# Performance work log

Measured on AMD Instinct MI355X. Metric: run time of the kernel, lower is better.

The kernel has to match this reference:

```python
import jax, jax.numpy as jnp
import numpy as np

D_MODEL = 1024
NUM_HEADS = 16
DEPTH = D_MODEL // NUM_HEADS


def setup_inputs() -> dict:
    key = jax.random.key(0)
    ks = jax.random.split(key, 11)
    B, S = 4, 2048
    scale = 1.0 / np.sqrt(D_MODEL)
    inp = {
        "q": jax.random.normal(ks[0], (B, S, D_MODEL), jnp.float32),
        "k": jax.random.normal(ks[1], (B, S, D_MODEL), jnp.float32),
        "v": jax.random.normal(ks[2], (B, S, D_MODEL), jnp.float32),
        # Linear params (weight stored [out, in] like torch; applied as x @ W.T + b)
        "wq_w": jax.random.normal(ks[3], (D_MODEL, D_MODEL), jnp.float32) * scale,
        "wq_b": jnp.zeros((D_MODEL,), jnp.float32),
        "wk_w": jax.random.normal(ks[4], (D_MODEL, D_MODEL), jnp.float32) * scale,
        "wk_b": jnp.zeros((D_MODEL,), jnp.float32),
        "wv_w": jax.random.normal(ks[5], (D_MODEL, D_MODEL), jnp.float32) * scale,
        "wv_b": jnp.zeros((D_MODEL,), jnp.float32),
        "wo_w": jax.random.normal(ks[6], (D_MODEL, D_MODEL), jnp.float32) * scale,
        "wo_b": jnp.zeros((D_MODEL,), jnp.float32),
    }
    return inp


def _split_heads(x, B, S):
    # [B, S, D] -> [B, H, S, depth]
    return x.reshape(B, S, NUM_HEADS, DEPTH).transpose(0, 2, 1, 3)


def reference(q, k, v, wq_w, wq_b, wk_w, wk_b, wv_w, wv_b, wo_w, wo_b):
    B, S, _ = q.shape
    qh = _split_heads(q @ wq_w.T + wq_b, B, S)
    kh = _split_heads(k @ wk_w.T + wk_b, B, S)
    vh = _split_heads(v @ wv_w.T + wv_b, B, S)
    # scaled dot-product attention: [B, H, Sq, Sk]
    scores = jnp.einsum("bhqd,bhkd->bhqk", qh, kh) / jnp.sqrt(
        jnp.asarray(DEPTH, qh.dtype))
    attn = jax.nn.softmax(scores, axis=-1)
    ctx = jnp.einsum("bhqk,bhkd->bhqd", attn, vh)
    # [B, H, S, depth] -> [B, S, D]
    ctx = ctx.transpose(0, 2, 1, 3).reshape(B, S, D_MODEL)
    return ctx @ wo_w.T + wo_b
```

## Files before the change

### kernel.cpp

```cpp
#include <hip/hip_runtime.h>
#include <hip/hip_bf16.h>

typedef __attribute__((ext_vector_type(8))) short bf16x8;
typedef __attribute__((ext_vector_type(4))) short bf16x4;
typedef __attribute__((ext_vector_type(4))) float f32x4;
typedef __attribute__((address_space(3))) ushort lds_ushort;

#define MFMA32(a, b, c) __builtin_amdgcn_mfma_f32_16x16x32_bf16(a, b, c, 0, 0, 0)
#if __has_builtin(__builtin_amdgcn_mfma_f32_16x16x16bf16_1k)
#define HAVE_MFMA16K 1
#define MFMA16K(a, b, c) __builtin_amdgcn_mfma_f32_16x16x16bf16_1k(a, b, c, 0, 0, 0)
#else
#define HAVE_MFMA16K 0
#endif

#define ASYNC16(g, l)                                                          \
    __builtin_amdgcn_global_load_lds(                                          \
        (const __attribute__((address_space(1))) unsigned int*)(g),            \
        (__attribute__((address_space(3))) unsigned int*)(l), 16, 0, 0)

#define TR16(dst, addr, OFF)                                                   \
    asm volatile("ds_read_b64_tr_b16 %0, %1 offset:%2"                         \
                 : "=v"(dst) : "v"(addr), "i"(OFF))

__device__ __forceinline__ ushort f2bf(float f) {
    __hip_bfloat16 h = __float2bfloat16(f);
    return *reinterpret_cast<ushort*>(&h);
}
__device__ __forceinline__ uint pack_bf16_2(float a, float b) {
    uint ua = __float_as_uint(a) + 0x8000u;
    uint ub = __float_as_uint(b) + 0x8000u;
    return (ua >> 16) | (ub & 0xFFFF0000u);
}

#define QSCALE 0.18033688011112042f

struct CvtArgs { const float* s[7]; ushort* d[7]; int nb[7]; };

__global__ __launch_bounds__(256) void cvtk(CvtArgs a) {
    const int z = blockIdx.y;
    if ((int)blockIdx.x >= a.nb[z]) return;
    const float* s = a.s[z];
    ushort* d = a.d[z];
    const size_t i = (size_t)blockIdx.x * 2048 + threadIdx.x * 8;
    float4 f0 = *(const float4*)&s[i];
    float4 f1 = *(const float4*)&s[i + 4];
    *(ushort4*)&d[i]     = make_ushort4(f2bf(f0.x), f2bf(f0.y), f2bf(f0.z), f2bf(f0.w));
    *(ushort4*)&d[i + 4] = make_ushort4(f2bf(f1.x), f2bf(f1.y), f2bf(f1.z), f2bf(f1.w));
}

struct GemmArgs {
    const ushort* X[3]; const ushort* W[3]; const float* B[3];
    void* O[3]; int mode[3]; float scale[3];
};

__global__ __launch_bounds__(256) void gemm3(GemmArgs g) {
    __shared__ __attribute__((aligned(16))) ushort As[2][128][32];
    __shared__ __attribute__((aligned(16))) ushort Bs[2][128][32];

    const int z = blockIdx.z;
    const ushort* __restrict__ X = g.X[z];
    const ushort* __restrict__ W = g.W[z];
    const float*  __restrict__ bias = g.B[z];
    const int mode = g.mode[z];
    const float scale = g.scale[z];

    const int tid  = threadIdx.x;
    const int lane = tid & 63;
    const int wave = tid >> 6;
    const int quad = lane >> 4;
    const int l16  = lane & 15;
    const int wm   = (wave >> 1) * 64;
    const int wn   = (wave & 1) * 64;

    const int flat = blockIdx.x + 8 * blockIdx.y;
    const int t    = (flat & 7) * 64 + (flat >> 3);
    const int m0   = (t >> 3) * 128;
    const int n0   = (t & 7) * 128;

    f32x4 acc[4][4];
#pragma unroll
    for (int i = 0; i < 4; i++)
#pragma unroll
        for (int j = 0; j < 4; j++) acc[i][j] = (f32x4)0.0f;

    auto stage = [&](int buf, int k0) {
#pragma unroll
        for (int j = 0; j < 2; j++) {
            const int c   = j * 256 + tid;
            const int r   = c >> 2;
            const int col = (c & 3) * 8;
            ASYNC16(&X[(size_t)(m0 + r) * 1024 + k0 + col],
                    &As[buf][0][0] + (size_t)(j * 256 + wave * 64) * 8);
            ASYNC16(&W[(size_t)(n0 + r) * 1024 + k0 + col],
                    &Bs[buf][0][0] + (size_t)(j * 256 + wave * 64) * 8);
        }
    };

    stage(0, 0);
    int cur = 0;

    for (int k0 = 0; k0 < 1024; k0 += 32) {
        __syncthreads();
        if (k0 + 32 < 1024) stage(cur ^ 1, k0 + 32);

        bf16x8 af[4], bfr[4];
#pragma unroll
        for (int i = 0; i < 4; i++)
            af[i] = *(const bf16x8*)&As[cur][wm + i * 16 + l16][quad * 8];
#pragma unroll
        for (int j = 0; j < 4; j++)
            bfr[j] = *(const bf16x8*)&Bs[cur][wn + j * 16 + l16][quad * 8];
#pragma unroll
        for (int i = 0; i < 4; i++)
#pragma unroll
            for (int j = 0; j < 4; j++)
                acc[i][j] = MFMA32(af[i], bfr[j], acc[i][j]);
        cur ^= 1;
    }

#pragma unroll
    for (int i = 0; i < 4; i++) {
#pragma unroll
        for (int j = 0; j < 4; j++) {
            const int n  = n0 + wn + j * 16 + l16;
            const float bb = bias[n];
#pragma unroll
            for (int r = 0; r < 4; r++) {
                const int m = m0 + wm + i * 16 + quad * 4 + r;
                const float val = (acc[i][j][r] + bb) * scale;
                if (mode == 2) {
                    ((float*)g.O[z])[(size_t)m * 1024 + n] = val;
                } else {
                    const int bat = m >> 11, s = m & 2047, h = n >> 6, d = n & 63;
                    ((ushort*)g.O[z])[((size_t)((bat * 16 + h) * 2048 + s)) * 64 + d]
                        = f2bf(val);
                }
            }
        }
    }
}

__global__ __launch_bounds__(256, 4) void attn(
    const ushort* __restrict__ Qp, const ushort* __restrict__ Kp,
    const ushort* __restrict__ Vp, ushort* __restrict__ ctx)
{
    __shared__ __attribute__((aligned(16))) ushort Ks[2][2 * 64 * 32];
    __shared__ __attribute__((aligned(16))) ushort Vs[2][64 * 64];

    const int tid  = threadIdx.x;
    const int lane = tid & 63;
    const int wave = tid >> 6;
    const int quad = lane >> 4;
    const int l16  = lane & 15;

    const int id = blockIdx.x;
    const int bh = (id & 7) * 8 + ((id >> 3) & 7);
    const int q0 = (id >> 6) * 128;
    const int b  = bh >> 4, h = bh & 15;

    const ushort* Qg = Qp + ((size_t)bh * 2048 + q0) * 64;
    const ushort* Kg = Kp + (size_t)bh * 2048 * 64;
    const ushort* Vg = Vp + (size_t)bh * 2048 * 64;

    bf16x8 aq[2][2];
#pragma unroll
    for (int st = 0; st < 2; st++)
#pragma unroll
        for (int kk = 0; kk < 2; kk++)
            aq[st][kk] = *(const bf16x8*)&Qg[(size_t)(wave * 32 + st * 16 + l16) * 64
                                            + kk * 32 + quad * 8];

    f32x4 o[2][4];
#pragma unroll
    for (int st = 0; st < 2; st++)
#pragma unroll
        for (int jd = 0; jd < 4; jd++) o[st][jd] = (f32x4)0.0f;
    float lsum[2] = {0.f, 0.f};

    auto stage = [&](int buf, int n0) {
#pragma unroll
        for (int j = 0; j < 2; j++) {
            const int c    = j * 256 + tid;
            const int colq = c & 3;
            const int row  = (c >> 2) & 63;
            const int half = c >> 8;
            ASYNC16(&Kg[(size_t)(n0 + row) * 64 + half * 32 + colq * 8],
                    &Ks[buf][0] + (size_t)(j * 256 + wave * 64) * 8);
        }
#pragma unroll
        for (int j = 0; j < 2; j++) {
            const int c   = j * 256 + tid;
            const int key = ((c >> 5) << 2) | ((c >> 1) & 3);
            const int d   = (((c >> 3) & 3) << 4) | ((c & 1) << 3);
            ASYNC16(&Vg[(size_t)(n0 + key) * 64 + d],
                    &Vs[buf][0] + (size_t)(j * 256 + wave * 64) * 8);
        }
    };

    stage(0, 0);
    int cur = 0;

    for (int n0 = 0; n0 < 2048; n0 += 64) {
        __syncthreads();
        if (n0 + 64 < 2048) stage(cur ^ 1, n0 + 64);

        uint pk[4][2][2];
#pragma unroll
        for (int kb = 0; kb < 4; kb++) {
            bf16x8 kf0 = *(const bf16x8*)&Ks[cur][(size_t)(kb * 16 + l16) * 32 + quad * 8];
            bf16x8 kf1 = *(const bf16x8*)&Ks[cur][(size_t)(64 + kb * 16 + l16) * 32 + quad * 8];
#pragma unroll
            for (int st = 0; st < 2; st++) {
                f32x4 s = (f32x4)0.0f;
                s = MFMA32(kf0, aq[st][0], s);
                s = MFMA32(kf1, aq[st][1], s);
                float e0 = __builtin_amdgcn_exp2f(s[0]);
                float e1 = __builtin_amdgcn_exp2f(s[1]);
                float e2 = __builtin_amdgcn_exp2f(s[2]);
                float e3 = __builtin_amdgcn_exp2f(s[3]);
                lsum[st] += (e0 + e1) + (e2 + e3);
                pk[kb][st][0] = pack_bf16_2(e0, e1);
                pk[kb][st][1] = pack_bf16_2(e2, e3);
            }
        }

#if HAVE_MFMA16K
        const lds_ushort* vp = (const lds_ushort*)&Vs[cur][0] + quad * 256 + l16 * 4;
        bf16x4 vf[4][4];
#define TRISSUE(JD)                                                            \
        TR16(vf[JD][0], vp, (JD) * 128 + 0);                                   \
        TR16(vf[JD][1], vp, (JD) * 128 + 2048);                                \
        TR16(vf[JD][2], vp, (JD) * 128 + 4096);                                \
        TR16(vf[JD][3], vp, (JD) * 128 + 6144);
        TRISSUE(0) TRISSUE(1) TRISSUE(2) TRISSUE(3)

#define PVWAIT(N)                                                              \
        asm volatile("s_waitcnt lgkmcnt(" #N ")" ::: "memory");                \
        __builtin_amdgcn_sched_barrier(0);
#define PVJD(JD)                                                               \
        _Pragma("unroll")                                                      \
        for (int kb = 0; kb < 4; kb++) {                                       \
            _Pragma("unroll")                                                  \
            for (int st = 0; st < 2; st++) {                                   \
                union { uint u[2]; bf16x4 v; } pf;                             \
                pf.u[0] = pk[kb][st][0];                                       \
                pf.u[1] = pk[kb][st][1];                                       \
                o[st][JD] = MFMA16K(pf.v, vf[JD][kb], o[st][JD]);              \
            }                                                                  \
        }
        __builtin_amdgcn_s_setprio(1);
        PVWAIT(12) PVJD(0)
        PVWAIT(8)  PVJD(1)
        PVWAIT(4)  PVJD(2)
        PVWAIT(0)  PVJD(3)
        __builtin_amdgcn_s_setprio(0);
#else
        const int addr0 = 4 * ((2 * (quad & 1)) * 16 + l16);
        const int addr1 = addr0 + 64;
#pragma unroll
        for (int kt = 0; kt < 2; kt++) {
            bf16x8 apf[2];
#pragma unroll
            for (int st = 0; st < 2; st++) {
                union { uint u[4]; bf16x8 v; } t;
#pragma unroll
                for (int j = 0; j < 4; j++) {
                    uint src = (quad & 2) ? pk[kt * 2 + 1][st][j & 1]
                                          : pk[kt * 2][st][j & 1];
                    t.u[j] = (uint)__builtin_amdgcn_ds_bpermute(
                        (j >> 1) ? addr1 : addr0, (int)src);
                }
                apf[st] = t.v;
            }
#pragma unroll
            for (int jd = 0; jd < 4; jd++) {
                union { ushort s[8]; bf16x8 v; } vv;
#pragma unroll
                for (int e = 0; e < 8; e++) {
                    const int key = kt * 32 + quad * 8 + e;
                    const int d   = jd * 16 + l16;
                    vv.s[e] = Vs[cur][(key >> 2) * 256 + (d >> 4) * 64
                                      + (key & 3) * 16 + (d & 15)];
                }
#pragma unroll
                for (int st = 0; st < 2; st++)
                    o[st][jd] = MFMA32(apf[st], vv.v, o[st][jd]);
            }
        }
#endif
        cur ^= 1;
    }

#pragma unroll
    for (int st = 0; st < 2; st++) {
        float ls = lsum[st];
        ls += __shfl_xor(ls, 16, 64);
        ls += __shfl_xor(ls, 32, 64);
        float inv[4];
#pragma unroll
        for (int r = 0; r < 4; r++)
            inv[r] = 1.0f / __shfl(ls, quad * 4 + r, 64);
#pragma unroll
        for (int jd = 0; jd < 4; jd++) {
#pragma unroll
            for (int r = 0; r < 4; r++) {
                const int s = q0 + wave * 32 + st * 16 + quad * 4 + r;
                ctx[((size_t)(b * 2048 + s)) * 1024 + h * 64 + jd * 16 + l16] =
                    f2bf(o[st][jd][r] * inv[r]);
            }
        }
    }
}

extern "C" void kernel_launch(void* const* d_in, const int* in_sizes, int n_in,
                              void* d_out, int out_size, void* d_ws, size_t ws_size,
                              hipStream_t stream) {
    const float* q    = (const float*)d_in[0];
    const float* k    = (const float*)d_in[1];
    const float* v    = (const float*)d_in[2];
    const float* wq_w = (const float*)d_in[3];
    const float* wq_b = (const float*)d_in[4];
    const float* wk_w = (const float*)d_in[5];
    const float* wk_b = (const float*)d_in[6];
    const float* wv_w = (const float*)d_in[7];
    const float* wv_b = (const float*)d_in[8];
    const float* wo_w = (const float*)d_in[9];
    const float* wo_b = (const float*)d_in[10];
    float* out = (float*)d_out;

    const size_t NE = (size_t)4 * 2048 * 1024;
    const size_t NW = (size_t)1024 * 1024;
    const size_t need_fused = (6 * NE + 4 * NW) * 2;

    dim3 blk(256);

    if (ws_size >= need_fused) {
        ushort* Xq = (ushort*)d_ws;
        ushort* Xk = Xq + NE;
        ushort* Xv = Xk + NE;
        ushort* Wq = Xv + NE;
        ushort* Wk = Wq + NW;
        ushort* Wv = Wk + NW;
        ushort* Wo = Wv + NW;
        ushort* Qp = Wo + NW;
        ushort* Kp = Qp + NE;
        ushort* Vp = Kp + NE;
        ushort* ctx = Xq;

        CvtArgs ca;
        ca.s[0]=q;    ca.d[0]=Xq; ca.nb[0]=4096;
        ca.s[1]=k;    ca.d[1]=Xk; ca.nb[1]=4096;
        ca.s[2]=v;    ca.d[2]=Xv; ca.nb[2]=4096;
        ca.s[3]=wq_w; ca.d[3]=Wq; ca.nb[3]=512;
        ca.s[4]=wk_w; ca.d[4]=Wk; ca.nb[4]=512;
        ca.s[5]=wv_w; ca.d[5]=Wv; ca.nb[5]=512;
        ca.s[6]=wo_w; ca.d[6]=Wo; ca.nb[6]=512;
        cvtk<<<dim3(4096, 7), blk, 0, stream>>>(ca);

        GemmArgs ga;
        ga.X[0]=Xq; ga.W[0]=Wq; ga.B[0]=wq_b; ga.O[0]=Qp; ga.mode[0]=0; ga.scale[0]=QSCALE;
        ga.X[1]=Xk; ga.W[1]=Wk; ga.B[1]=wk_b; ga.O[1]=Kp; ga.mode[1]=0; ga.scale[1]=1.0f;
        ga.X[2]=Xv; ga.W[2]=Wv; ga.B[2]=wv_b; ga.O[2]=Vp; ga.mode[2]=0; ga.scale[2]=1.0f;
        gemm3<<<dim3(8, 64, 3), blk, 0, stream>>>(ga);

        attn<<<dim3(1024), blk, 0, stream>>>(Qp, Kp, Vp, ctx);

        GemmArgs go;
        go.X[0]=ctx; go.W[0]=Wo; go.B[0]=wo_b; go.O[0]=out; go.mode[0]=2; go.scale[0]=1.0f;
        go.X[1]=go.X[0]; go.W[1]=go.W[0]; go.B[1]=go.B[0]; go.O[1]=go.O[0]; go.mode[1]=2; go.scale[1]=1.0f;
        go.X[2]=go.X[0]; go.W[2]=go.W[0]; go.B[2]=go.B[0]; go.O[2]=go.O[0]; go.mode[2]=2; go.scale[2]=1.0f;
        gemm3<<<dim3(8, 64, 1), blk, 0, stream>>>(go);
    } else {
        ushort* Xb  = (ushort*)d_ws;
        ushort* Wb  = Xb + NE;
        ushort* Wob = Wb + NW;
        ushort* Qp  = Wob + NW;
        ushort* Kp  = Qp + NE;
        ushort* Vp  = Kp + NE;
        ushort* ctx = Xb;

        CvtArgs c0;
        c0.s[0]=q;    c0.d[0]=Xb;  c0.nb[0]=4096;
        c0.s[1]=wq_w; c0.d[1]=Wb;  c0.nb[1]=512;
        c0.s[2]=wo_w; c0.d[2]=Wob; c0.nb[2]=512;
        for (int i = 3; i < 7; i++) { c0.s[i]=q; c0.d[i]=Xb; c0.nb[i]=0; }
        cvtk<<<dim3(4096, 3), blk, 0, stream>>>(c0);
        GemmArgs ga;
        for (int i = 0; i < 3; i++) { ga.X[i]=Xb; ga.W[i]=Wb; ga.B[i]=wq_b; ga.O[i]=Qp; ga.mode[i]=0; ga.scale[i]=QSCALE; }
        gemm3<<<dim3(8, 64, 1), blk, 0, stream>>>(ga);

        CvtArgs c1;
        c1.s[0]=k;    c1.d[0]=Xb; c1.nb[0]=4096;
        c1.s[1]=wk_w; c1.d[1]=Wb; c1.nb[1]=512;
        for (int i = 2; i < 7; i++) { c1.s[i]=k; c1.d[i]=Xb; c1.nb[i]=0; }
        cvtk<<<dim3(4096, 2), blk, 0, stream>>>(c1);
        GemmArgs gb;
        for (int i = 0; i < 3; i++) { gb.X[i]=Xb; gb.W[i]=Wb; gb.B[i]=wk_b; gb.O[i]=Kp; gb.mode[i]=0; gb.scale[i]=1.0f; }
        gemm3<<<dim3(8, 64, 1), blk, 0, stream>>>(gb);

        CvtArgs c2;
        c2.s[0]=v;    c2.d[0]=Xb; c2.nb[0]=4096;
        c2.s[1]=wv_w; c2.d[1]=Wb; c2.nb[1]=512;
        for (int i = 2; i < 7; i++) { c2.s[i]=v; c2.d[i]=Xb; c2.nb[i]=0; }
        cvtk<<<dim3(4096, 2), blk, 0, stream>>>(c2);
        GemmArgs gc;
        for (int i = 0; i < 3; i++) { gc.X[i]=Xb; gc.W[i]=Wb; gc.B[i]=wv_b; gc.O[i]=Vp; gc.mode[i]=0; gc.scale[i]=1.0f; }
        gemm3<<<dim3(8, 64, 1), blk, 0, stream>>>(gc);

        attn<<<dim3(1024), blk, 0, stream>>>(Qp, Kp, Vp, ctx);

        GemmArgs go;
        for (int i = 0; i < 3; i++) { go.X[i]=ctx; go.W[i]=Wob; go.B[i]=wo_b; go.O[i]=out; go.mode[i]=2; go.scale[i]=1.0f; }
        gemm3<<<dim3(8, 64, 1), blk, 0, stream>>>(go);
    }
}
```

Before: 350.8 us.

## Deepen GEMM prefetch pipeline, use MFMA for softmax row sums, hardware bf16 pack

The projection GEMM now prefetches two K-tiles ahead. It uses explicit vmcnt waits and split barriers so the next load is issued right after the fragments are read into registers, which should overlap global loads with MFMA compute. In the attention kernel, the softmax denominator is now accumulated with an MFMA against a ones vector instead of scalar adds and cross-lane shuffles. That MFMA sums the bf16-rounded probabilities, which slightly changes numerics. Packing the exponentials to bf16 now uses the v_cvt_pk_bf16_f32 instruction in place of the manual integer rounding.

```diff
diff --git a/kernel.cpp b/kernel.cpp
--- a/kernel.cpp
+++ b/kernel.cpp
@@ -27,10 +27,10 @@
     __hip_bfloat16 h = __float2bfloat16(f);
     return *reinterpret_cast<ushort*>(&h);
 }
-__device__ __forceinline__ uint pack_bf16_2(float a, float b) {
-    uint ua = __float_as_uint(a) + 0x8000u;
-    uint ub = __float_as_uint(b) + 0x8000u;
-    return (ua >> 16) | (ub & 0xFFFF0000u);
+__device__ __forceinline__ uint cvtpk(float a, float b) {
+    uint r;
+    asm("v_cvt_pk_bf16_f32 %0, %1, %2" : "=v"(r) : "v"(a), "v"(b));
+    return r;
 }
 
 #define QSCALE 0.18033688011112042f
@@ -98,11 +98,17 @@
     };
 
     stage(0, 0);
+    stage(1, 32);
     int cur = 0;
 
     for (int k0 = 0; k0 < 1024; k0 += 32) {
-        __syncthreads();
-        if (k0 + 32 < 1024) stage(cur ^ 1, k0 + 32);
+        if (k0 < 1024 - 32) {
+            asm volatile("s_waitcnt vmcnt(4)" ::: "memory");
+        } else {
+            asm volatile("s_waitcnt vmcnt(0)" ::: "memory");
+        }
+        __builtin_amdgcn_s_barrier();
+        __builtin_amdgcn_sched_barrier(0);
 
         bf16x8 af[4], bfr[4];
 #pragma unroll
@@ -111,6 +117,12 @@
 #pragma unroll
         for (int j = 0; j < 4; j++)
             bfr[j] = *(const bf16x8*)&Bs[cur][wn + j * 16 + l16][quad * 8];
+        asm volatile("s_waitcnt lgkmcnt(0)" ::: "memory");
+        __builtin_amdgcn_sched_barrier(0);
+        __builtin_amdgcn_s_barrier();
+        __builtin_amdgcn_sched_barrier(0);
+        if (k0 + 64 < 1024) stage(cur, k0 + 64);
+
 #pragma unroll
         for (int i = 0; i < 4; i++)
 #pragma unroll
@@ -176,7 +188,13 @@
     for (int st = 0; st < 2; st++)
 #pragma unroll
         for (int jd = 0; jd < 4; jd++) o[st][jd] = (f32x4)0.0f;
+#if HAVE_MFMA16K
+    f32x4 ls[2] = {(f32x4)0.0f, (f32x4)0.0f};
+    union { uint u[2]; bf16x4 v; } ones;
+    ones.u[0] = 0x3F803F80u; ones.u[1] = 0x3F803F80u;
+#else
     float lsum[2] = {0.f, 0.f};
+#endif
 
     auto stage = [&](int buf, int n0) {
 #pragma unroll
@@ -219,9 +237,11 @@
                 float e1 = __builtin_amdgcn_exp2f(s[1]);
                 float e2 = __builtin_amdgcn_exp2f(s[2]);
                 float e3 = __builtin_amdgcn_exp2f(s[3]);
+                pk[kb][st][0] = cvtpk(e0, e1);
+                pk[kb][st][1] = cvtpk(e2, e3);
+#if !HAVE_MFMA16K
                 lsum[st] += (e0 + e1) + (e2 + e3);
-                pk[kb][st][0] = pack_bf16_2(e0, e1);
-                pk[kb][st][1] = pack_bf16_2(e2, e3);
+#endif
             }
         }
 
@@ -234,6 +254,17 @@
         TR16(vf[JD][2], vp, (JD) * 128 + 4096);                                \
         TR16(vf[JD][3], vp, (JD) * 128 + 6144);
         TRISSUE(0) TRISSUE(1) TRISSUE(2) TRISSUE(3)
+
+#pragma unroll
+        for (int kb = 0; kb < 4; kb++) {
+#pragma unroll
+            for (int st = 0; st < 2; st++) {
+                union { uint u[2]; bf16x4 v; } pf;
+                pf.u[0] = pk[kb][st][0];
+                pf.u[1] = pk[kb][st][1];
+                ls[st] = MFMA16K(pf.v, ones.v, ls[st]);
+            }
+        }
 
 #define PVWAIT(N)                                                              \
         asm volatile("s_waitcnt lgkmcnt(" #N ")" ::: "memory");                \
@@ -292,15 +323,12 @@
         cur ^= 1;
     }
 
+#if HAVE_MFMA16K
 #pragma unroll
     for (int st = 0; st < 2; st++) {
-        float ls = lsum[st];
-        ls += __shfl_xor(ls, 16, 64);
-        ls += __shfl_xor(ls, 32, 64);
         float inv[4];
 #pragma unroll
-        for (int r = 0; r < 4; r++)
-            inv[r] = 1.0f / __shfl(ls, quad * 4 + r, 64);
+        for (int r = 0; r < 4; r++) inv[r] = 1.0f / ls[st][r];
 #pragma unroll
         for (int jd = 0; jd < 4; jd++) {
 #pragma unroll
@@ -311,6 +339,27 @@
             }
         }
     }
+#else
+#pragma unroll
+    for (int st = 0; st < 2; st++) {
+        float lsv = lsum[st];
+        lsv += __shfl_xor(lsv, 16, 64);
+        lsv += __shfl_xor(lsv, 32, 64);
+        float inv[4];
+#pragma unroll
+        for (int r = 0; r < 4; r++)
+            inv[r] = 1.0f / __shfl(lsv, quad * 4 + r, 64);
+#pragma unroll
+        for (int jd = 0; jd < 4; jd++) {
+#pragma unroll
+            for (int r = 0; r < 4; r++) {
+                const int s = q0 + wave * 32 + st * 16 + quad * 4 + r;
+                ctx[((size_t)(b * 2048 + s)) * 1024 + h * 64 + jd * 16 + l16] =
+                    f2bf(o[st][jd][r] * inv[r]);
+            }
+        }
+    }
+#endif
 }
 
 extern "C" void kernel_launch(void* const* d_in, const int* in_sizes, int n_in,
```

New measurement: 338.4 us. 1.04x faster.
